# Performance work log

Hardware: AMD Instinct MI355X
Metric: run time of the kernel (lower is better)

Reference implementation:

```python
import jax, jax.numpy as jnp
import numpy as np
from jax import lax

N = 64          # n (even -> odd=0, add_odd=0)
B = 256         # batch
F = 256         # input_features
ITERS = 10      # sinkhorn iterations


def _conv1d(x, w, b, pad, dil):
    # x: (B, Cin, L), w: (Cout, Cin, K) torch layout
    y = lax.conv_general_dilated(
        x, w, window_strides=(1,), padding=[(pad, pad)],
        rhs_dilation=(dil,), dimension_numbers=("NCH", "OIH", "NCH"))
    return y + b[None, :, None]


def setup_inputs() -> dict:
    key = jax.random.key(0)
    ks = jax.random.split(key, 17)
    s = 0.02
    d = {
        "x": jax.random.normal(ks[0], (B, F), jnp.float32),
        # linear stack (torch Linear layout: (out, in))
        "w1": jax.random.normal(ks[1], (2 * N, F), jnp.float32) * s,
        "b1": jax.random.normal(ks[2], (2 * N,), jnp.float32) * s,
        "w2": jax.random.normal(ks[3], (N * N, 2 * N), jnp.float32) * s,
        "b2": jax.random.normal(ks[4], (N * N,), jnp.float32) * s,
        "w3": jax.random.normal(ks[5], (4 * N * N, N * N), jnp.float32) * s,
        "b3": jax.random.normal(ks[6], (4 * N * N,), jnp.float32) * s,
        # conv stack: 2n->3n->2n->n->n->n, all k=3
        "cw1": jax.random.normal(ks[7], (3 * N, 2 * N, 3), jnp.float32) * s,
        "cb1": jax.random.normal(ks[8], (3 * N,), jnp.float32) * s,
        "cw2": jax.random.normal(ks[9], (2 * N, 3 * N, 3), jnp.float32) * s,
        "cb2": jax.random.normal(ks[10], (2 * N,), jnp.float32) * s,
        "cw3": jax.random.normal(ks[11], (N, 2 * N, 3), jnp.float32) * s,
        "cb3": jax.random.normal(ks[12], (N,), jnp.float32) * s,
        "cw4": jax.random.normal(ks[13], (N, N, 3), jnp.float32) * s,
        "cb4": jax.random.normal(ks[14], (N,), jnp.float32) * s,
        "cw5": jax.random.normal(ks[15], (N, N, 3), jnp.float32) * s,
        "cb5": jax.random.normal(ks[16], (N,), jnp.float32) * s,
    }
    return d


def _sink(x, iters):
    # output = x + 0.001; repeat: row-normalize then col-normalize
    out = x + 0.001

    def body(o, _):
        o = o / jnp.sum(o, axis=2, keepdims=True)  # row_sink: divide each row by its sum
        o = o / jnp.sum(o, axis=1, keepdims=True)  # col_sink: divide each column by its sum
        return o, None

    out, _ = lax.scan(body, out, None, length=iters)
    return out


def reference(x, w1, b1, w2, b2, w3, b3,
              cw1, cb1, cw2, cb2, cw3, cb3, cw4, cb4, cw5, cb5):
    h = x @ w1.T + b1
    h = h @ w2.T + b2
    h = h @ w3.T + b3                      # (B, 4n^2)
    h = h.reshape(B, 2 * N, 2 * N)         # (B, 128, 128)
    # conv1: p=0, d=(n-8)//2=28 (since n>10); rest pad=0, dil=1
    h = _conv1d(h, cw1, cb1, 0, (N - 8) // 2)  # (B, 192, 72)
    h = _conv1d(h, cw2, cb2, 0, 1)             # (B, 128, 70)
    h = _conv1d(h, cw3, cb3, 0, 1)             # (B, 64, 68)
    h = _conv1d(h, cw4, cb4, 0, 1)             # (B, 64, 66)
    h = _conv1d(h, cw5, cb5, 0, 1)             # (B, 64, 64)
    h = h * h                                   # torch.pow(x, 2)
    return _sink(h, ITERS)
```

## Files before the change

kernel.cpp:

```cpp
#include <hip/hip_runtime.h>
#include <hip/hip_bf16.h>

typedef float f32x4 __attribute__((ext_vector_type(4)));
typedef __bf16 bf16x8 __attribute__((ext_vector_type(8)));

typedef __attribute__((address_space(1))) const unsigned int as1_uint;
typedef __attribute__((address_space(3))) unsigned int as3_uint;

__global__ __launch_bounds__(128) void gemm1_k(const float* __restrict__ x,
                                               const float* __restrict__ w1,
                                               const float* __restrict__ b1,
                                               float* __restrict__ h1) {
    __shared__ float xs[256];
    const int m = blockIdx.x, t = threadIdx.x;
    xs[t] = x[m * 256 + t];
    xs[t + 128] = x[m * 256 + 128 + t];
    __syncthreads();
    float acc = b1[t];
    const float4* wr = (const float4*)(w1 + t * 256);
#pragma unroll 8
    for (int k4 = 0; k4 < 64; ++k4) {
        float4 w = wr[k4];
        acc += xs[k4 * 4 + 0] * w.x + xs[k4 * 4 + 1] * w.y +
               xs[k4 * 4 + 2] * w.z + xs[k4 * 4 + 3] * w.w;
    }
    h1[m * 128 + t] = acc;
}

__global__ __launch_bounds__(256) void gemm2_k(const float* __restrict__ h1,
                                               const float* __restrict__ w2,
                                               const float* __restrict__ b2,
                                               char* __restrict__ h2b) {
    __shared__ float As[64][129];
    __shared__ float Bs[64][129];
    const int nb = blockIdx.x, mb = blockIdx.y, t = threadIdx.x;
#pragma unroll
    for (int i = 0; i < 8; ++i) {
        int idx = i * 256 + t;
        int row = idx >> 5, c4 = (idx & 31) * 4;
        float4 a = *(const float4*)(h1 + (mb * 64 + row) * 128 + c4);
        As[row][c4 + 0] = a.x; As[row][c4 + 1] = a.y;
        As[row][c4 + 2] = a.z; As[row][c4 + 3] = a.w;
        float4 bv = *(const float4*)(w2 + (nb * 64 + row) * 128 + c4);
        Bs[row][c4 + 0] = bv.x; Bs[row][c4 + 1] = bv.y;
        Bs[row][c4 + 2] = bv.z; Bs[row][c4 + 3] = bv.w;
    }
    __syncthreads();
    const int tx = t & 15, ty = t >> 4;
    float acc[4][4] = {};
#pragma unroll 4
    for (int k = 0; k < 128; ++k) {
        float a[4], b[4];
#pragma unroll
        for (int i = 0; i < 4; ++i) a[i] = As[ty * 4 + i][k];
#pragma unroll
        for (int j = 0; j < 4; ++j) b[j] = Bs[tx * 4 + j][k];
#pragma unroll
        for (int i = 0; i < 4; ++i)
#pragma unroll
            for (int j = 0; j < 4; ++j) acc[i][j] += a[i] * b[j];
    }
#pragma unroll
    for (int i = 0; i < 4; ++i)
#pragma unroll
        for (int j = 0; j < 4; ++j) {
            int m = mb * 64 + ty * 4 + i;
            int n = nb * 64 + tx * 4 + j;
            float v = acc[i][j] + b2[n];
            int kb = n >> 6, r = n & 63;
            int byte = kb * 32768 + ((m * 128 + (r >> 3) * 16) ^ ((m & 7) << 4)) + (r & 7) * 2;
            *(__bf16*)(h2b + byte) = (__bf16)v;
        }
}

__global__ __launch_bounds__(512, 1) void gemm3_k(const char* __restrict__ Ab,
                                                  const float* __restrict__ W,
                                                  const float* __restrict__ bias,
                                                  float* __restrict__ C) {
    __shared__ __align__(16) char lds[81920];
    const int tid = threadIdx.x;
    const int n0 = blockIdx.x * 64;
    const int lane = tid & 63, wid = tid >> 6;
    const int mrow = tid >> 3, kb8 = tid & 7;

#define ISSUE_A(t, buf)                                                          \
    {                                                                            \
        const char* _s = Ab + (t) * 32768 + wid * 4096 + lane * 16;              \
        char* _d = lds + (buf) * 32768 + wid * 4096;                             \
        __builtin_amdgcn_global_load_lds((as1_uint*)(_s), (as3_uint*)(_d), 16, 0, 0);          \
        __builtin_amdgcn_global_load_lds((as1_uint*)(_s + 1024), (as3_uint*)(_d + 1024), 16, 0, 0); \
        __builtin_amdgcn_global_load_lds((as1_uint*)(_s + 2048), (as3_uint*)(_d + 2048), 16, 0, 0); \
        __builtin_amdgcn_global_load_lds((as1_uint*)(_s + 3072), (as3_uint*)(_d + 3072), 16, 0, 0); \
    }

    float4 w0, w1;
    auto loadW = [&](int t) {
        const float* q = W + (n0 + mrow) * 4096 + t * 64 + kb8 * 8;
        w0 = *(const float4*)q;
        w1 = *(const float4*)(q + 4);
    };
    auto storeW = [&](int buf) {
        bf16x8 p;
        p[0] = (__bf16)w0.x; p[1] = (__bf16)w0.y; p[2] = (__bf16)w0.z; p[3] = (__bf16)w0.w;
        p[4] = (__bf16)w1.x; p[5] = (__bf16)w1.y; p[6] = (__bf16)w1.z; p[7] = (__bf16)w1.w;
        *(bf16x8*)(lds + 65536 + buf * 8192 +
                   ((mrow * 128 + kb8 * 16) ^ ((mrow & 7) << 4))) = p;
    };

    ISSUE_A(0, 0);
    loadW(0);
    __syncthreads();
    storeW(0);
    __syncthreads();

    const int lr = lane & 15, lq = lane >> 4;
    const int wm = wid >> 1, wn = wid & 1;

    f32x4 acc[4][2];
    const f32x4 zero = {0.f, 0.f, 0.f, 0.f};
#pragma unroll
    for (int mi = 0; mi < 4; ++mi)
#pragma unroll
        for (int ni = 0; ni < 2; ++ni) acc[mi][ni] = zero;

    for (int t = 0; t < 64; ++t) {
        const int cur = t & 1;
        if (t < 63) {
            ISSUE_A(t + 1, cur ^ 1);
            loadW(t + 1);
        }
        const char* Ac = lds + cur * 32768;
        const char* Wc = lds + 65536 + cur * 8192;
#pragma unroll
        for (int kk = 0; kk < 2; ++kk) {
            const int kb = kk * 4 + lq;
            bf16x8 af[4], bfv[2];
#pragma unroll
            for (int mi = 0; mi < 4; ++mi) {
                int m = wm * 64 + mi * 16 + lr;
                af[mi] = *(const bf16x8*)(Ac + ((m * 128 + kb * 16) ^ ((m & 7) << 4)));
            }
#pragma unroll
            for (int ni = 0; ni < 2; ++ni) {
                int n = wn * 32 + ni * 16 + lr;
                bfv[ni] = *(const bf16x8*)(Wc + ((n * 128 + kb * 16) ^ ((n & 7) << 4)));
            }
#pragma unroll
            for (int mi = 0; mi < 4; ++mi)
#pragma unroll
                for (int ni = 0; ni < 2; ++ni)
                    acc[mi][ni] = __builtin_amdgcn_mfma_f32_16x16x32_bf16(
                        af[mi], bfv[ni], acc[mi][ni], 0, 0, 0);
        }
        __syncthreads();
        if (t < 63) storeW(cur ^ 1);
        __syncthreads();
    }
#undef ISSUE_A

    float bv[2];
#pragma unroll
    for (int ni = 0; ni < 2; ++ni) bv[ni] = bias[n0 + wn * 32 + ni * 16 + lr];
#pragma unroll
    for (int mi = 0; mi < 4; ++mi)
#pragma unroll
        for (int ni = 0; ni < 2; ++ni) {
            const int n = n0 + wn * 32 + ni * 16 + lr;
#pragma unroll
            for (int r = 0; r < 4; ++r) {
                int m = wm * 64 + mi * 16 + lq * 4 + r;
                C[m * 16384 + n] = acc[mi][ni][r] + bv[ni];
            }
        }
}

template <int CIN, int COUT, int DIL, int MT, int NT>
__device__ __forceinline__ void conv_core(const char* xt, char* wl,
                                          const float* __restrict__ w,
                                          f32x4 (&acc)[MT][NT], int tid) {
    constexpr int RB = CIN * 2;
    const int lane = tid & 63, wid = tid >> 6;
    const int lr = lane & 15, lq = lane >> 4;
    const int cobase = wid * (COUT / 4);
    const f32x4 zero = {0.f, 0.f, 0.f, 0.f};
#pragma unroll
    for (int mi = 0; mi < MT; ++mi)
#pragma unroll
        for (int ni = 0; ni < NT; ++ni) acc[mi][ni] = zero;

    for (int cic = 0; cic < CIN / 32; ++cic) {
        for (int idx = tid; idx < COUT * 4; idx += 256) {
            int co = idx >> 2, cib = idx & 3, ci0 = cic * 32 + cib * 8;
            const float* src = w + co * (CIN * 3) + ci0 * 3;
            float v[24];
#pragma unroll
            for (int u = 0; u < 6; ++u) {
                float4 f = *(const float4*)(src + u * 4);
                v[u * 4 + 0] = f.x; v[u * 4 + 1] = f.y;
                v[u * 4 + 2] = f.z; v[u * 4 + 3] = f.w;
            }
#pragma unroll
            for (int tp = 0; tp < 3; ++tp) {
                bf16x8 pk;
#pragma unroll
                for (int j = 0; j < 8; ++j) pk[j] = (__bf16)v[j * 3 + tp];
                *(bf16x8*)(wl + ((tp * 4 + cib) * COUT + co) * 16) = pk;
            }
        }
        __syncthreads();
#pragma unroll
        for (int tp = 0; tp < 3; ++tp) {
            bf16x8 af[MT];
#pragma unroll
            for (int mi = 0; mi < MT; ++mi)
                af[mi] = *(const bf16x8*)(wl + ((tp * 4 + lq) * COUT + cobase + mi * 16 + lr) * 16);
            bf16x8 bfr[NT];
#pragma unroll
            for (int ni = 0; ni < NT; ++ni) {
                int colX = ni * 16 + lr + tp * DIL;
                bfr[ni] = *(const bf16x8*)(xt + ((colX * RB + (cic * 4 + lq) * 16) ^ ((colX & 7) << 4)));
            }
#pragma unroll
            for (int mi = 0; mi < MT; ++mi)
#pragma unroll
                for (int ni = 0; ni < NT; ++ni)
                    acc[mi][ni] = __builtin_amdgcn_mfma_f32_16x16x32_bf16(
                        af[mi], bfr[ni], acc[mi][ni], 0, 0, 0);
        }
        __syncthreads();
    }
}

template <int COUT, int LOUT, int MT, int NT>
__device__ __forceinline__ void write_xt(char* xt_out, const f32x4 (&acc)[MT][NT],
                                         const float* __restrict__ bias, int tid) {
    constexpr int RBO = COUT * 2;
    const int lane = tid & 63, wid = tid >> 6;
    const int lr = lane & 15, lq = lane >> 4;
    const int cobase = wid * (COUT / 4);
#pragma unroll
    for (int mi = 0; mi < MT; ++mi)
#pragma unroll
        for (int ni = 0; ni < NT; ++ni) {
            int l = ni * 16 + lr;
            if (l < LOUT) {
#pragma unroll
                for (int r = 0; r < 4; ++r) {
                    int co = cobase + mi * 16 + lq * 4 + r;
                    float y = acc[mi][ni][r] + bias[co];
                    int byte = (l * RBO + ((co >> 3) << 4) + (co & 7) * 2) ^ ((l & 7) << 4);
                    *(__bf16*)(xt_out + byte) = (__bf16)y;
                }
            }
        }
}

__global__ __launch_bounds__(256, 1) void convsink_k(
    const float* __restrict__ h3,
    const float* __restrict__ cw1, const float* __restrict__ cb1,
    const float* __restrict__ cw2, const float* __restrict__ cb2,
    const float* __restrict__ cw3, const float* __restrict__ cb3,
    const float* __restrict__ cw4, const float* __restrict__ cb4,
    const float* __restrict__ cw5, const float* __restrict__ cb5,
    float* __restrict__ out) {
    __shared__ __align__(16) char lds[34816 + 31488 + 36864 + 16640];
    char* xtA = lds;
    char* xtB = lds + 34816;
    char* wl = lds + 34816 + 31488;
    float* S = (float*)(lds + 34816 + 31488 + 36864);

    const int b = blockIdx.x, tid = threadIdx.x;
    const float* src = h3 + b * 16384;

#pragma unroll
    for (int i = 0; i < 8; ++i) {
        int idx = i * 256 + tid;
        int l = idx & 127, cib = idx >> 7;
        bf16x8 p;
#pragma unroll
        for (int j = 0; j < 8; ++j) p[j] = (__bf16)src[(cib * 8 + j) * 128 + l];
        *(bf16x8*)(xtA + ((l * 256 + cib * 16) ^ ((l & 7) << 4))) = p;
    }
    __syncthreads();

    {
        f32x4 acc[3][5];
        conv_core<128, 192, 28, 3, 5>(xtA, wl, cw1, acc, tid);
        write_xt<192, 72, 3, 5>(xtB, acc, cb1, tid);
    }
    __syncthreads();
    {
        f32x4 acc[2][5];
        conv_core<192, 128, 1, 2, 5>(xtB, wl, cw2, acc, tid);
        write_xt<128, 70, 2, 5>(xtA, acc, cb2, tid);
    }
    __syncthreads();
    {
        f32x4 acc[1][5];
        conv_core<128, 64, 1, 1, 5>(xtA, wl, cw3, acc, tid);
        write_xt<64, 68, 1, 5>(xtB, acc, cb3, tid);
    }
    __syncthreads();
    {
        f32x4 acc[1][5];
        conv_core<64, 64, 1, 1, 5>(xtB, wl, cw4, acc, tid);
        write_xt<64, 66, 1, 5>(xtA, acc, cb4, tid);
    }
    __syncthreads();
    {
        f32x4 acc[1][4];
        conv_core<64, 64, 1, 1, 4>(xtA, wl, cw5, acc, tid);
        const int lane = tid & 63, wid = tid >> 6;
        const int lr = lane & 15, lq = lane >> 4;
        const int cobase = wid * 16;
#pragma unroll
        for (int ni = 0; ni < 4; ++ni) {
            int l = ni * 16 + lr;
#pragma unroll
            for (int r = 0; r < 4; ++r) {
                int co = cobase + lq * 4 + r;
                float y = acc[0][ni][r] + cb5[co];
                S[co * 65 + l] = y * y + 0.001f;
            }
        }
    }
    __syncthreads();

    const int q = tid & 3, rid = tid >> 2;
    for (int it = 0; it < 10; ++it) {
        float p = 0.f;
#pragma unroll
        for (int j = 0; j < 16; ++j) p += S[rid * 65 + q * 16 + j];
        p += __shfl_xor(p, 1);
        p += __shfl_xor(p, 2);
        float inv = 1.0f / p;
#pragma unroll
        for (int j = 0; j < 16; ++j) S[rid * 65 + q * 16 + j] *= inv;
        __syncthreads();
        float c = 0.f;
#pragma unroll
        for (int i = 0; i < 16; ++i) c += S[(q * 16 + i) * 65 + rid];
        c += __shfl_xor(c, 1);
        c += __shfl_xor(c, 2);
        float invc = 1.0f / c;
#pragma unroll
        for (int i = 0; i < 16; ++i) S[(q * 16 + i) * 65 + rid] *= invc;
        __syncthreads();
    }

#pragma unroll
    for (int i = 0; i < 16; ++i) {
        int idx = i * 256 + tid;
        out[b * 4096 + idx] = S[(idx >> 6) * 65 + (idx & 63)];
    }
}

extern "C" void kernel_launch(void* const* d_in, const int* in_sizes, int n_in,
                              void* d_out, int out_size, void* d_ws, size_t ws_size,
                              hipStream_t stream) {
    const float* x = (const float*)d_in[0];
    const float* w1 = (const float*)d_in[1];
    const float* b1 = (const float*)d_in[2];
    const float* w2 = (const float*)d_in[3];
    const float* b2 = (const float*)d_in[4];
    const float* w3 = (const float*)d_in[5];
    const float* b3 = (const float*)d_in[6];
    const float* cw1 = (const float*)d_in[7];
    const float* cb1 = (const float*)d_in[8];
    const float* cw2 = (const float*)d_in[9];
    const float* cb2 = (const float*)d_in[10];
    const float* cw3 = (const float*)d_in[11];
    const float* cb3 = (const float*)d_in[12];
    const float* cw4 = (const float*)d_in[13];
    const float* cb4 = (const float*)d_in[14];
    const float* cw5 = (const float*)d_in[15];
    const float* cb5 = (const float*)d_in[16];
    float* out = (float*)d_out;

    char* ws = (char*)d_ws;
    float* h1 = (float*)(ws);
    char* h2b = ws + 131072;
    float* h3 = (float*)(ws + 131072 + 2097152);

    gemm1_k<<<256, 128, 0, stream>>>(x, w1, b1, h1);
    gemm2_k<<<dim3(64, 4), 256, 0, stream>>>(h1, w2, b2, h2b);
    gemm3_k<<<256, 512, 0, stream>>>(h2b, w3, b3, h3);
    convsink_k<<<256, 256, 0, stream>>>(h3, cw1, cb1, cw2, cb2, cw3, cb3,
                                        cw4, cb4, cw5, cb5, out);
}
```

Before: 150.1 us.

## Stream fp32 W tiles directly to LDS and use triple-buffered async pipeline in gemm3

The gemm3 kernel now loads the fp32 weight tiles straight into LDS with global_load_lds, using an XOR swizzle, instead of loading them into registers, converting to bf16 and storing. Conversion to bf16 moves to fragment-read time. Both A and W tiles are now triple-buffered, prefetched two steps ahead, and guarded by explicit vmcnt waits with one barrier per iteration instead of two. This removes the register round trip and a barrier, at the cost of a larger LDS footprint (144KB), twice the LDS traffic for W, and conversion work repeated by every wave.

Measured after the change: 156.8 us. 1.04x slower.

```diff
diff --git a/kernel.cpp b/kernel.cpp
--- a/kernel.cpp
+++ b/kernel.cpp
@@ -77,45 +77,38 @@
                                                   const float* __restrict__ W,
                                                   const float* __restrict__ bias,
                                                   float* __restrict__ C) {
-    __shared__ __align__(16) char lds[81920];
+    __shared__ __align__(16) char lds[147456];
     const int tid = threadIdx.x;
     const int n0 = blockIdx.x * 64;
     const int lane = tid & 63, wid = tid >> 6;
-    const int mrow = tid >> 3, kb8 = tid & 7;
-
-#define ISSUE_A(t, buf)                                                          \
-    {                                                                            \
-        const char* _s = Ab + (t) * 32768 + wid * 4096 + lane * 16;              \
-        char* _d = lds + (buf) * 32768 + wid * 4096;                             \
-        __builtin_amdgcn_global_load_lds((as1_uint*)(_s), (as3_uint*)(_d), 16, 0, 0);          \
-        __builtin_amdgcn_global_load_lds((as1_uint*)(_s + 1024), (as3_uint*)(_d + 1024), 16, 0, 0); \
-        __builtin_amdgcn_global_load_lds((as1_uint*)(_s + 2048), (as3_uint*)(_d + 2048), 16, 0, 0); \
-        __builtin_amdgcn_global_load_lds((as1_uint*)(_s + 3072), (as3_uint*)(_d + 3072), 16, 0, 0); \
-    }
-
-    float4 w0, w1;
-    auto loadW = [&](int t) {
-        const float* q = W + (n0 + mrow) * 4096 + t * 64 + kb8 * 8;
-        w0 = *(const float4*)q;
-        w1 = *(const float4*)(q + 4);
-    };
-    auto storeW = [&](int buf) {
-        bf16x8 p;
-        p[0] = (__bf16)w0.x; p[1] = (__bf16)w0.y; p[2] = (__bf16)w0.z; p[3] = (__bf16)w0.w;
-        p[4] = (__bf16)w1.x; p[5] = (__bf16)w1.y; p[6] = (__bf16)w1.z; p[7] = (__bf16)w1.w;
-        *(bf16x8*)(lds + 65536 + buf * 8192 +
-                   ((mrow * 128 + kb8 * 16) ^ ((mrow & 7) << 4))) = p;
-    };
-
-    ISSUE_A(0, 0);
-    loadW(0);
-    __syncthreads();
-    storeW(0);
-    __syncthreads();
-
     const int lr = lane & 15, lq = lane >> 4;
     const int wm = wid >> 1, wn = wid & 1;
 
+    const char* Asrc = Ab + wid * 4096 + lane * 16;
+
+    const int n_a = wid * 4 + (lane >> 4);
+    const int n_b = 32 + n_a;
+    const int g_d = lane & 15;
+    const int sw_a = ((n_a & 7) << 1) | ((n_a >> 3) & 1);
+    const int sw_b = ((n_b & 7) << 1) | ((n_b >> 3) & 1);
+    const char* WsrcA = (const char*)W + (size_t)(n0 + n_a) * 16384 + (g_d ^ sw_a) * 16;
+    const char* WsrcB = (const char*)W + (size_t)(n0 + n_b) * 16384 + (g_d ^ sw_b) * 16;
+
+#define ISSUE(kt, s)                                                                  \
+    {                                                                                 \
+        const char* _a = Asrc + (size_t)(kt) * 32768;                                 \
+        char* _ad = lds + (s) * 32768 + wid * 4096;                                   \
+        __builtin_amdgcn_global_load_lds((as1_uint*)(_a), (as3_uint*)(_ad), 16, 0, 0);              \
+        __builtin_amdgcn_global_load_lds((as1_uint*)(_a + 1024), (as3_uint*)(_ad + 1024), 16, 0, 0);  \
+        __builtin_amdgcn_global_load_lds((as1_uint*)(_a + 2048), (as3_uint*)(_ad + 2048), 16, 0, 0);  \
+        __builtin_amdgcn_global_load_lds((as1_uint*)(_a + 3072), (as3_uint*)(_ad + 3072), 16, 0, 0);  \
+        const char* _wa = WsrcA + (size_t)(kt) * 256;                                 \
+        const char* _wb = WsrcB + (size_t)(kt) * 256;                                 \
+        char* _wd = lds + 98304 + (s) * 16384 + wid * 1024;                           \
+        __builtin_amdgcn_global_load_lds((as1_uint*)(_wa), (as3_uint*)(_wd), 16, 0, 0);             \
+        __builtin_amdgcn_global_load_lds((as1_uint*)(_wb), (as3_uint*)(_wd + 8192), 16, 0, 0);      \
+    }
+
     f32x4 acc[4][2];
     const f32x4 zero = {0.f, 0.f, 0.f, 0.f};
 #pragma unroll
@@ -123,14 +116,19 @@
 #pragma unroll
         for (int ni = 0; ni < 2; ++ni) acc[mi][ni] = zero;
 
-    for (int t = 0; t < 64; ++t) {
-        const int cur = t & 1;
-        if (t < 63) {
-            ISSUE_A(t + 1, cur ^ 1);
-            loadW(t + 1);
-        }
-        const char* Ac = lds + cur * 32768;
-        const char* Wc = lds + 65536 + cur * 8192;
+    const int nfr[2] = {wn * 32 + lr, wn * 32 + 16 + lr};
+    int wfr[2][2];
+#pragma unroll
+    for (int ni = 0; ni < 2; ++ni) {
+        int n = nfr[ni];
+        int s_n = ((n & 7) << 1) | ((n >> 3) & 1);
+        wfr[ni][0] = n * 256 + (s_n ^ 0) * 0;
+        wfr[ni][1] = s_n;
+    }
+
+    auto mfma_tile = [&](int s) {
+        const char* Ac = lds + s * 32768;
+        const char* Wc = lds + 98304 + s * 16384;
 #pragma unroll
         for (int kk = 0; kk < 2; ++kk) {
             const int kb = kk * 4 + lq;
@@ -142,8 +140,15 @@
             }
 #pragma unroll
             for (int ni = 0; ni < 2; ++ni) {
-                int n = wn * 32 + ni * 16 + lr;
-                bfv[ni] = *(const bf16x8*)(Wc + ((n * 128 + kb * 16) ^ ((n & 7) << 4)));
+                int n = nfr[ni];
+                int s_n = wfr[ni][1];
+                int g0 = kb * 2;
+                float4 f0 = *(const float4*)(Wc + n * 256 + ((g0 ^ s_n) * 16));
+                float4 f1 = *(const float4*)(Wc + n * 256 + (((g0 + 1) ^ s_n) * 16));
+                bf16x8 p;
+                p[0] = (__bf16)f0.x; p[1] = (__bf16)f0.y; p[2] = (__bf16)f0.z; p[3] = (__bf16)f0.w;
+                p[4] = (__bf16)f1.x; p[5] = (__bf16)f1.y; p[6] = (__bf16)f1.z; p[7] = (__bf16)f1.w;
+                bfv[ni] = p;
             }
 #pragma unroll
             for (int mi = 0; mi < 4; ++mi)
@@ -152,11 +157,31 @@
                     acc[mi][ni] = __builtin_amdgcn_mfma_f32_16x16x32_bf16(
                         af[mi], bfv[ni], acc[mi][ni], 0, 0, 0);
         }
-        __syncthreads();
-        if (t < 63) storeW(cur ^ 1);
-        __syncthreads();
-    }
-#undef ISSUE_A
+    };
+
+    ISSUE(0, 0);
+    ISSUE(1, 1);
+    asm volatile("s_waitcnt vmcnt(6)" ::: "memory");
+    __builtin_amdgcn_sched_barrier(0);
+    __builtin_amdgcn_s_barrier();
+
+    int s = 0;
+#pragma unroll 1
+    for (int t = 0; t < 64; ++t) {
+        int s2 = s + 2;
+        if (s2 >= 3) s2 -= 3;
+        if (t < 62) ISSUE(t + 2, s2);
+        mfma_tile(s);
+        if (t < 62) {
+            asm volatile("s_waitcnt vmcnt(6)" ::: "memory");
+        } else if (t == 62) {
+            asm volatile("s_waitcnt vmcnt(0)" ::: "memory");
+        }
+        __builtin_amdgcn_sched_barrier(0);
+        if (t < 63) __builtin_amdgcn_s_barrier();
+        s = (s == 2) ? 0 : s + 1;
+    }
+#undef ISSUE
 
     float bv[2];
 #pragma unroll
```

## Warp-specialize gemm3 with producer waves and 3-stage LDS flag pipeline

Applied to the files above, without the earlier changes.

Restructures the third GEMM kernel so that two extra producer waves issue async global-to-LDS loads for both A and the fp32 W tile into a triple-buffered LDS ring. Eight consumer waves wait on LDS flags instead of block-wide barriers, and they convert W to bf16 at fragment-read time. The goal is to overlap memory traffic with MFMA work and remove the per-iteration __syncthreads and register staging of W. In exchange, W now sits in LDS as fp32, which doubles its footprint, and the spin-wait polling with s_sleep adds latency and risks hangs or ordering bugs.

Result: no change. 150.5 us (+0.3%).

```diff
diff --git a/kernel.cpp b/kernel.cpp
--- a/kernel.cpp
+++ b/kernel.cpp
@@ -6,6 +6,10 @@
 
 typedef __attribute__((address_space(1))) const unsigned int as1_uint;
 typedef __attribute__((address_space(3))) unsigned int as3_uint;
+
+__device__ __forceinline__ void pollGE(volatile int* p, int v) {
+    while (*p < v) __builtin_amdgcn_s_sleep(1);
+}
 
 __global__ __launch_bounds__(128) void gemm1_k(const float* __restrict__ x,
                                                const float* __restrict__ w1,
@@ -73,105 +77,143 @@
         }
 }
 
-__global__ __launch_bounds__(512, 1) void gemm3_k(const char* __restrict__ Ab,
+__global__ __launch_bounds__(640, 1) void gemm3_k(const char* __restrict__ Ab,
                                                   const float* __restrict__ W,
                                                   const float* __restrict__ bias,
                                                   float* __restrict__ C) {
-    __shared__ __align__(16) char lds[81920];
+    __shared__ __align__(16) char lds[147456];
+    __shared__ int flagA[3], flagB[3], doneC[3];
     const int tid = threadIdx.x;
     const int n0 = blockIdx.x * 64;
     const int lane = tid & 63, wid = tid >> 6;
-    const int mrow = tid >> 3, kb8 = tid & 7;
-
-#define ISSUE_A(t, buf)                                                          \
-    {                                                                            \
-        const char* _s = Ab + (t) * 32768 + wid * 4096 + lane * 16;              \
-        char* _d = lds + (buf) * 32768 + wid * 4096;                             \
-        __builtin_amdgcn_global_load_lds((as1_uint*)(_s), (as3_uint*)(_d), 16, 0, 0);          \
-        __builtin_amdgcn_global_load_lds((as1_uint*)(_s + 1024), (as3_uint*)(_d + 1024), 16, 0, 0); \
-        __builtin_amdgcn_global_load_lds((as1_uint*)(_s + 2048), (as3_uint*)(_d + 2048), 16, 0, 0); \
-        __builtin_amdgcn_global_load_lds((as1_uint*)(_s + 3072), (as3_uint*)(_d + 3072), 16, 0, 0); \
-    }
-
-    float4 w0, w1;
-    auto loadW = [&](int t) {
-        const float* q = W + (n0 + mrow) * 4096 + t * 64 + kb8 * 8;
-        w0 = *(const float4*)q;
-        w1 = *(const float4*)(q + 4);
-    };
-    auto storeW = [&](int buf) {
-        bf16x8 p;
-        p[0] = (__bf16)w0.x; p[1] = (__bf16)w0.y; p[2] = (__bf16)w0.z; p[3] = (__bf16)w0.w;
-        p[4] = (__bf16)w1.x; p[5] = (__bf16)w1.y; p[6] = (__bf16)w1.z; p[7] = (__bf16)w1.w;
-        *(bf16x8*)(lds + 65536 + buf * 8192 +
-                   ((mrow * 128 + kb8 * 16) ^ ((mrow & 7) << 4))) = p;
-    };
-
-    ISSUE_A(0, 0);
-    loadW(0);
-    __syncthreads();
-    storeW(0);
-    __syncthreads();
-
-    const int lr = lane & 15, lq = lane >> 4;
-    const int wm = wid >> 1, wn = wid & 1;
-
-    f32x4 acc[4][2];
-    const f32x4 zero = {0.f, 0.f, 0.f, 0.f};
-#pragma unroll
-    for (int mi = 0; mi < 4; ++mi)
-#pragma unroll
-        for (int ni = 0; ni < 2; ++ni) acc[mi][ni] = zero;
-
-    for (int t = 0; t < 64; ++t) {
-        const int cur = t & 1;
-        if (t < 63) {
-            ISSUE_A(t + 1, cur ^ 1);
-            loadW(t + 1);
-        }
-        const char* Ac = lds + cur * 32768;
-        const char* Wc = lds + 65536 + cur * 8192;
-#pragma unroll
-        for (int kk = 0; kk < 2; ++kk) {
-            const int kb = kk * 4 + lq;
-            bf16x8 af[4], bfv[2];
-#pragma unroll
-            for (int mi = 0; mi < 4; ++mi) {
-                int m = wm * 64 + mi * 16 + lr;
-                af[mi] = *(const bf16x8*)(Ac + ((m * 128 + kb * 16) ^ ((m & 7) << 4)));
-            }
+
+    if (tid == 0) {
+#pragma unroll
+        for (int i = 0; i < 3; ++i) { flagA[i] = 0; flagB[i] = 0; doneC[i] = 0; }
+    }
+    __syncthreads();
+
+    if (wid >= 8) {
+        const int p = wid - 8;
+        volatile int* myflag = (p == 0) ? flagA : flagB;
+
+        const char* Abase = Ab + p * 16384 + lane * 16;
+        const char* Wb8 = (const char*)W;
+        const char* wsrc[8];
+        int wdst[8];
+#pragma unroll
+        for (int j = 0; j < 8; ++j) {
+            int gi = p * 512 + j * 64 + lane;
+            int row = gi >> 4, dseg = gi & 15;
+            int sseg = dseg ^ (((row & 7) << 1) | ((row >> 3) & 1));
+            wsrc[j] = Wb8 + (size_t)(n0 + row) * 16384 + sseg * 16;
+            wdst[j] = row * 256 + dseg * 16;
+        }
+
+#define ISSUE_P(kt, s)                                                                   \
+    {                                                                                    \
+        const char* _a = Abase + (size_t)(kt) * 32768;                                   \
+        char* _ad = lds + (s) * 49152 + p * 16384;                                       \
+        _Pragma("unroll") for (int i = 0; i < 16; ++i)                                   \
+            __builtin_amdgcn_global_load_lds((as1_uint*)(_a + i * 1024),                 \
+                                             (as3_uint*)(_ad + i * 1024), 16, 0, 0);     \
+        char* _wd = lds + (s) * 49152 + 32768;                                           \
+        _Pragma("unroll") for (int j = 0; j < 8; ++j)                                    \
+            __builtin_amdgcn_global_load_lds((as1_uint*)(wsrc[j] + (size_t)(kt) * 256),  \
+                                             (as3_uint*)(_wd + wdst[j]), 16, 0, 0);      \
+    }
+
+#pragma unroll 1
+        for (int t = 0; t < 64; ++t) {
+            const int s = t % 3, u = t / 3;
+            if (u > 0) pollGE((volatile int*)&doneC[s], 8 * u);
+            __builtin_amdgcn_sched_barrier(0);
+            ISSUE_P(t, s);
+            if (t >= 1) {
+                asm volatile("s_waitcnt vmcnt(24)" ::: "memory");
+                __builtin_amdgcn_sched_barrier(0);
+                myflag[(t - 1) % 3] = (t - 1) / 3 + 1;
+            }
+        }
+        asm volatile("s_waitcnt vmcnt(0)" ::: "memory");
+        __builtin_amdgcn_sched_barrier(0);
+        myflag[63 % 3] = 63 / 3 + 1;
+#undef ISSUE_P
+    } else {
+        const int lr = lane & 15, lq = lane >> 4;
+        const int wm = wid >> 1, wn = wid & 1;
+
+        f32x4 acc[4][2];
+        const f32x4 zero = {0.f, 0.f, 0.f, 0.f};
+#pragma unroll
+        for (int mi = 0; mi < 4; ++mi)
+#pragma unroll
+            for (int ni = 0; ni < 2; ++ni) acc[mi][ni] = zero;
+
+        const int nf0 = wn * 32 + lr, nf1 = wn * 32 + 16 + lr;
+        const int sw0 = ((nf0 & 7) << 1) | ((nf0 >> 3) & 1);
+        const int sw1 = ((nf1 & 7) << 1) | ((nf1 >> 3) & 1);
+
+#pragma unroll 1
+        for (int t = 0; t < 64; ++t) {
+            const int s = t % 3, u = t / 3;
+            pollGE((volatile int*)&flagA[s], u + 1);
+            pollGE((volatile int*)&flagB[s], u + 1);
+            __builtin_amdgcn_sched_barrier(0);
+
+            const char* Ac = lds + s * 49152;
+            const char* Wc = Ac + 32768;
+#pragma unroll
+            for (int kk = 0; kk < 2; ++kk) {
+                const int kb = kk * 4 + lq;
+                bf16x8 af[4], bfv[2];
+#pragma unroll
+                for (int mi = 0; mi < 4; ++mi) {
+                    int m = wm * 64 + mi * 16 + lr;
+                    af[mi] = *(const bf16x8*)(Ac + ((m * 128 + kb * 16) ^ ((m & 7) << 4)));
+                }
+                {
+                    float4 f0 = *(const float4*)(Wc + nf0 * 256 + (((2 * kb) ^ sw0) << 4));
+                    float4 f1 = *(const float4*)(Wc + nf0 * 256 + (((2 * kb + 1) ^ sw0) << 4));
+                    bf16x8 pk;
+                    pk[0] = (__bf16)f0.x; pk[1] = (__bf16)f0.y; pk[2] = (__bf16)f0.z; pk[3] = (__bf16)f0.w;
+                    pk[4] = (__bf16)f1.x; pk[5] = (__bf16)f1.y; pk[6] = (__bf16)f1.z; pk[7] = (__bf16)f1.w;
+                    bfv[0] = pk;
+                }
+                {
+                    float4 f0 = *(const float4*)(Wc + nf1 * 256 + (((2 * kb) ^ sw1) << 4));
+                    float4 f1 = *(const float4*)(Wc + nf1 * 256 + (((2 * kb + 1) ^ sw1) << 4));
+                    bf16x8 pk;
+                    pk[0] = (__bf16)f0.x; pk[1] = (__bf16)f0.y; pk[2] = (__bf16)f0.z; pk[3] = (__bf16)f0.w;
+                    pk[4] = (__bf16)f1.x; pk[5] = (__bf16)f1.y; pk[6] = (__bf16)f1.z; pk[7] = (__bf16)f1.w;
+                    bfv[1] = pk;
+                }
+#pragma unroll
+                for (int mi = 0; mi < 4; ++mi)
+#pragma unroll
+                    for (int ni = 0; ni < 2; ++ni)
+                        acc[mi][ni] = __builtin_amdgcn_mfma_f32_16x16x32_bf16(
+                            af[mi], bfv[ni], acc[mi][ni], 0, 0, 0);
+            }
+            __builtin_amdgcn_sched_barrier(0);
+            if (lane == 0) atomicAdd(&doneC[s], 1);
+        }
+
+        float bv[2];
+#pragma unroll
+        for (int ni = 0; ni < 2; ++ni) bv[ni] = bias[n0 + wn * 32 + ni * 16 + lr];
+#pragma unroll
+        for (int mi = 0; mi < 4; ++mi)
 #pragma unroll
             for (int ni = 0; ni < 2; ++ni) {
-                int n = wn * 32 + ni * 16 + lr;
-                bfv[ni] = *(const bf16x8*)(Wc + ((n * 128 + kb * 16) ^ ((n & 7) << 4)));
-            }
-#pragma unroll
-            for (int mi = 0; mi < 4; ++mi)
-#pragma unroll
-                for (int ni = 0; ni < 2; ++ni)
-                    acc[mi][ni] = __builtin_amdgcn_mfma_f32_16x16x32_bf16(
-                        af[mi], bfv[ni], acc[mi][ni], 0, 0, 0);
-        }
-        __syncthreads();
-        if (t < 63) storeW(cur ^ 1);
-        __syncthreads();
-    }
-#undef ISSUE_A
-
-    float bv[2];
-#pragma unroll
-    for (int ni = 0; ni < 2; ++ni) bv[ni] = bias[n0 + wn * 32 + ni * 16 + lr];
-#pragma unroll
-    for (int mi = 0; mi < 4; ++mi)
-#pragma unroll
-        for (int ni = 0; ni < 2; ++ni) {
-            const int n = n0 + wn * 32 + ni * 16 + lr;
-#pragma unroll
-            for (int r = 0; r < 4; ++r) {
-                int m = wm * 64 + mi * 16 + lq * 4 + r;
-                C[m * 16384 + n] = acc[mi][ni][r] + bv[ni];
-            }
-        }
+                const int n = n0 + wn * 32 + ni * 16 + lr;
+#pragma unroll
+                for (int r = 0; r < 4; ++r) {
+                    int m = wm * 64 + mi * 16 + lq * 4 + r;
+                    C[m * 16384 + n] = acc[mi][ni][r] + bv[ni];
+                }
+            }
+    }
 }
 
 template <int CIN, int COUT, int DIL, int MT, int NT>
@@ -384,7 +426,7 @@
 
     gemm1_k<<<256, 128, 0, stream>>>(x, w1, b1, h1);
     gemm2_k<<<dim3(64, 4), 256, 0, stream>>>(h1, w2, b2, h2b);
-    gemm3_k<<<256, 512, 0, stream>>>(h2b, w3, b3, h3);
+    gemm3_k<<<256, 640, 0, stream>>>(h2b, w3, b3, h3);
     convsink_k<<<256, 256, 0, stream>>>(h3, cw1, cb1, cw2, cb2, cw3, cb3,
                                         cw4, cb4, cw5, cb5, out);
 }
```
